# Kernel optimization log

Measured on AMD Instinct MI355X. Metric: run time of the kernel, lower is better.

Reference implementation:

```python
import jax, jax.numpy as jnp
import numpy as np

N = 20000
E = 320000
NEG_SLOPE = 0.2
LN_EPS = 1e-5


def gat_conv(x, W, a_src, a_dst, b, src, dst, heads, ch, concat):
    # x: [N, F_in]; W: [F_in, H*C]; a_src/a_dst: [H, C]; b: [H*C] or [C]
    xl = (x @ W).reshape(N, heads, ch)                      # [N,H,C]
    alpha_src = jnp.sum(xl * a_src, axis=-1)                # [N,H]
    alpha_dst = jnp.sum(xl * a_dst, axis=-1)                # [N,H]
    e = alpha_src[src] + alpha_dst[dst]                     # [E',H]
    e = jax.nn.leaky_relu(e, NEG_SLOPE)
    # segment softmax over incoming edges of each dst node
    m = jax.ops.segment_max(e, dst, num_segments=N)         # [N,H]
    m = jnp.where(jnp.isfinite(m), m, 0.0)
    ex = jnp.exp(e - m[dst])
    denom = jax.ops.segment_sum(ex, dst, num_segments=N)    # [N,H]
    alpha = ex / (denom[dst] + 1e-16)                       # [E',H]
    msg = alpha[:, :, None] * xl[src]                       # [E',H,C]
    out = jax.ops.segment_sum(msg, dst, num_segments=N)     # [N,H,C]
    if concat:
        return out.reshape(N, heads * ch) + b
    return out.mean(axis=1) + b


def layer_norm(x, g, b):
    mu = jnp.mean(x, axis=-1, keepdims=True)
    var = jnp.mean(jnp.square(x - mu), axis=-1, keepdims=True)
    return (x - mu) * jax.lax.rsqrt(var + LN_EPS) * g + b


def setup_inputs() -> dict:
    key = jax.random.key(0)
    ks = jax.random.split(key, 24)
    d = {}
    d["x"] = jax.random.normal(ks[0], (N, 50), dtype=jnp.float32)
    d["edge_index"] = jax.random.randint(ks[1], (2, E), 0, N, dtype=jnp.int64)

    def glorot(k, shape):
        fan = shape[0] + shape[-1]
        return jax.random.normal(k, shape, dtype=jnp.float32) * np.sqrt(2.0 / fan)

    # conv1: 50 -> 256, heads=4, concat
    d["W1"] = glorot(ks[2], (50, 4 * 256))
    d["a_src1"] = glorot(ks[3], (4, 256))
    d["a_dst1"] = glorot(ks[4], (4, 256))
    d["b1"] = jnp.zeros((4 * 256,), jnp.float32)
    # conv2: 1024 -> 256, heads=4, concat
    d["W2"] = glorot(ks[5], (1024, 4 * 256))
    d["a_src2"] = glorot(ks[6], (4, 256))
    d["a_dst2"] = glorot(ks[7], (4, 256))
    d["b2"] = jnp.zeros((4 * 256,), jnp.float32)
    # conv3: 1024 -> 121, heads=6, concat=False
    d["W3"] = glorot(ks[8], (1024, 6 * 121))
    d["a_src3"] = glorot(ks[9], (6, 121))
    d["a_dst3"] = glorot(ks[10], (6, 121))
    d["b3"] = jnp.zeros((121,), jnp.float32)
    # skips
    d["skipW1"] = glorot(ks[11], (50, 1024))
    d["skipb1"] = jnp.zeros((1024,), jnp.float32)
    d["skipW2"] = glorot(ks[12], (1024, 1024))
    d["skipb2"] = jnp.zeros((1024,), jnp.float32)
    # layer norms
    d["g1"] = jnp.ones((1024,), jnp.float32)
    d["beta1"] = jnp.zeros((1024,), jnp.float32)
    d["g2"] = jnp.ones((1024,), jnp.float32)
    d["beta2"] = jnp.zeros((1024,), jnp.float32)
    return d


def reference(x, edge_index, W1, a_src1, a_dst1, b1, W2, a_src2, a_dst2, b2,
              W3, a_src3, a_dst3, b3, skipW1, skipb1, skipW2, skipb2,
              g1, beta1, g2, beta2):
    # add self loops (PyG GATConv default)
    loop = jnp.arange(N, dtype=edge_index.dtype)
    src = jnp.concatenate([edge_index[0], loop])
    dst = jnp.concatenate([edge_index[1], loop])

    h = gat_conv(x, W1, a_src1, a_dst1, b1, src, dst, 4, 256, True)
    h = jax.nn.elu(layer_norm(h + (x @ skipW1 + skipb1), g1, beta1))
    h2 = gat_conv(h, W2, a_src2, a_dst2, b2, src, dst, 4, 256, True)
    h2 = jax.nn.elu(layer_norm(h2 + (h @ skipW2 + skipb2), g2, beta2))
    out = gat_conv(h2, W3, a_src3, a_dst3, b3, src, dst, 6, 121, False)
    return out
```

## Files before the change

kernel.cpp:

```cpp
#include <hip/hip_runtime.h>
#include <hip/hip_bf16.h>
#include <math.h>

typedef __attribute__((ext_vector_type(8))) __bf16 bf16x8;
typedef __attribute__((ext_vector_type(4))) float f32x4;

#define MPAD 20224
#define SSZ ((size_t)MPAD * 128)

#if __has_builtin(__builtin_amdgcn_global_load_lds)
#define GLD16(g, l)                                                                      \
    __builtin_amdgcn_global_load_lds(                                                    \
        (const __attribute__((address_space(1))) unsigned int*)(g),                      \
        (__attribute__((address_space(3))) unsigned int*)(l), 16, 0, 0)
#else
#define GLD16(g, l) (*(bf16x8*)(l) = *(const bf16x8*)(g))
#endif

#define BAR() asm volatile("s_barrier" ::: "memory")
#define WAITVM(N) asm volatile("s_waitcnt vmcnt(" #N ")" ::: "memory")


#define STAGE_T(t_)                                                                      \
    do {                                                                                 \
        __bf16* Ld = lds + (((t_) & 3) * 16384);                                         \
        const __bf16* Ga = Abase + (t_) * 32;                                            \
        const __bf16* Gb = Bbase + (t_) * 32;                                            \
        GLD16(Ga, Ld + tt * 8);                                                          \
        GLD16(Ga + (size_t)128 * K_, Ld + (tt + 512) * 8);                               \
        GLD16(Gb, Ld + 8192 + tt * 8);                                                   \
        GLD16(Gb + (size_t)128 * K_, Ld + 8192 + (tt + 512) * 8);                        \
    } while (0)

#define LOAD_FRAGS(t_)                                                                   \
    {                                                                                    \
        const __bf16* Ar = lds + (((t_) & 3) * 16384) + aoff;                            \
        const __bf16* Br = lds + (((t_) & 3) * 16384) + 8192 + boff;                     \
        _Pragma("unroll") for (int i = 0; i < 8; i++)                                    \
            af[i] = *(const bf16x8*)(Ar + i * 512);                                      \
        _Pragma("unroll") for (int j = 0; j < 4; j++)                                    \
            bf[j] = *(const bf16x8*)(Br + j * 512);                                      \
    }

#define MFMA_ALL()                                                                       \
    __builtin_amdgcn_s_setprio(1);                                                       \
    _Pragma("unroll") for (int i = 0; i < 8; i++)                                        \
        _Pragma("unroll") for (int j = 0; j < 4; j++)                                    \
            acc[i][j] = __builtin_amdgcn_mfma_f32_16x16x32_bf16(af[i], bf[j],            \
                                                                acc[i][j], 0, 0, 0);     \
    __builtin_amdgcn_s_setprio(0);

#define GEMM256_BODY(A, Bt, K_, ...)                                                     \
    __shared__ __align__(16) __bf16 lds[65536];                                          \
    const int tt = threadIdx.x;                                                          \
    const int lane = tt & 63;                                                            \
    const int wid = tt >> 6;                                                             \
    const int wr = wid >> 2;                                           \
    const int wc = wid & 3;                                         \
     \
    const int nwg = gridDim.x * gridDim.y;                                               \
    const int wg0 = blockIdx.y * gridDim.x + blockIdx.x;                                 \
    const int qq = nwg >> 3, rr = nwg & 7, xcd = wg0 & 7, oo = wg0 >> 3;                 \
    const int swz = (xcd < rr ? xcd * (qq + 1) : rr * (qq + 1) + (xcd - rr) * qq) + oo;  \
    const int bm = (swz / gridDim.x) * 256;                                              \
    const int bn = (swz % gridDim.x) * 256;                                              \
    const int m16 = lane & 15;                                                           \
    const int c4 = lane >> 4;                                                            \
    const int NT = K_ >> 5;                                                              \
    const int ttp = tt ^ (((tt >> 5) & 1) << 1);          \
    const int srow = ttp >> 2;                                                           \
    const int sch = (ttp & 3) << 3;                                                      \
    const __bf16* Abase = A + (size_t)(bm + srow) * K_ + sch;                            \
    const __bf16* Bbase = Bt + (size_t)(bn + srow) * K_ + sch;                           \
    const int fsw = ((m16 >> 3) & 1) << 4;                                               \
    const int aoff = (((wr * 128 + m16) * 32) + c4 * 8) ^ fsw;                           \
    const int boff = (((wc * 64 + m16) * 32) + c4 * 8) ^ fsw;                            \
    f32x4 acc[8][4];                                                                     \
    _Pragma("unroll") for (int i = 0; i < 8; i++)                                        \
        _Pragma("unroll") for (int j = 0; j < 4; j++)                                    \
            acc[i][j] = (f32x4){0.f, 0.f, 0.f, 0.f};                                     \
    bf16x8 af[8], bf[4];                                                                 \
                      \
    STAGE_T(0);                                                                          \
    if (NT > 1) STAGE_T(1);                                                              \
    if (NT > 2) STAGE_T(2);                                                              \
    if (NT > 2) { WAITVM(8); } else if (NT > 1) { WAITVM(4); } else { WAITVM(0); }       \
    BAR();                                                                               \
    for (int t = 0; t < NT; t++) {                                                       \
        if (t + 3 < NT) STAGE_T(t + 3);                                                  \
        LOAD_FRAGS(t);                                                                   \
        MFMA_ALL();                                                                      \
        if (t + 1 < NT) {                                                                \
            if (t + 3 < NT) { WAITVM(8); }                                               \
            else if (t + 3 == NT) { WAITVM(4); }                                         \
            else { WAITVM(0); }                                                          \
            BAR();                                                                       \
        }                                                                                \
    }                                                                                    \
    __VA_ARGS__

__global__ __launch_bounds__(512, 2) void gemm256_bt(const __bf16* __restrict__ A,
                                                     const __bf16* __restrict__ Bt,
                                                     __bf16* __restrict__ C,
                                                     int M, int N_, int K_) {
    GEMM256_BODY(A, Bt, K_,
        { const int r4 = c4 << 2;
          const int rb = bm + wr * 128;
          _Pragma("unroll") for (int i = 0; i < 8; i++)
              _Pragma("unroll") for (int j = 0; j < 4; j++) {
                  int col = bn + wc * 64 + j * 16 + m16;
                  size_t sb_ = (size_t)(col >> 7) * SSZ + (col & 127);
                  _Pragma("unroll") for (int r = 0; r < 4; r++) {
                      int row = rb + i * 16 + r4 + r;
                      C[sb_ + (size_t)row * 128] = (__bf16)acc[i][j][r];
                  }
              } })
}

__global__ __launch_bounds__(512, 2) void gemm256_bt2(const __bf16* __restrict__ A,
                                                      const __bf16* __restrict__ Bt,
                                                      __bf16* __restrict__ C0,
                                                      __bf16* __restrict__ C1,
                                                      int M, int K_) {
    GEMM256_BODY(A, Bt, K_,
        { const int r4 = c4 << 2;
          const int rb = bm + wr * 128;
          _Pragma("unroll") for (int i = 0; i < 8; i++)
              _Pragma("unroll") for (int j = 0; j < 4; j++) {
                  int col = bn + wc * 64 + j * 16 + m16;
                  __bf16* Cp = (col < 1024) ? C0 : C1;
                  int c10 = col & 1023;
                  size_t sb_ = (size_t)(c10 >> 7) * SSZ + (c10 & 127);
                  _Pragma("unroll") for (int r = 0; r < 4; r++) {
                      int row = rb + i * 16 + r4 + r;
                      Cp[sb_ + (size_t)row * 128] = (__bf16)acc[i][j][r];
                  }
              } })
}

__device__ __forceinline__ void transpose_tile(const float* __restrict__ W,
                                               __bf16* __restrict__ WT,
                                               int K, int N, int Kp, int Np,
                                               int bx, int by, float* sm) {
    int tx = threadIdx.x & 31, ty = threadIdx.x >> 5;
#pragma unroll
    for (int r = ty; r < 32; r += 8) {
        int k = by * 32 + r, n = bx * 32 + tx;
        float v = 0.f;
        if (k < K && n < N) v = W[(size_t)k * N + n];
        sm[r * 33 + tx] = v;
    }
    __syncthreads();
#pragma unroll
    for (int r = ty; r < 32; r += 8) {
        int n = bx * 32 + r, k = by * 32 + tx;
        if (n < Np && k < Kp) WT[(size_t)n * Kp + k] = (__bf16)sm[tx * 33 + r];
    }
}

__device__ __forceinline__ void transpose_w3_tile(const float* __restrict__ W,
                                                  __bf16* __restrict__ WT,
                                                  int bx, int by, float* sm) {
    int tx = threadIdx.x & 31, ty = threadIdx.x >> 5;
    int r0 = bx * 32;
    int h = r0 >> 7;
    int c0 = r0 & 127;
#pragma unroll
    for (int r = ty; r < 32; r += 8) {
        int k = by * 32 + r;
        int c = c0 + tx;
        float v = 0.f;
        if (c < 121) v = W[(size_t)k * 726 + h * 121 + c];
        sm[r * 33 + tx] = v;
    }
    __syncthreads();
#pragma unroll
    for (int r = ty; r < 32; r += 8) {
        int rr = r0 + r;
        int k = by * 32 + tx;
        WT[(size_t)rr * 1024 + k] = (__bf16)sm[tx * 33 + r];
    }
}

__global__ __launch_bounds__(256) void prep_k(const float* __restrict__ x,
                                              const float* __restrict__ W1,
                                              const float* __restrict__ sW1,
                                              const float* __restrict__ W2,
                                              const float* __restrict__ sW2,
                                              const float* __restrict__ W3,
                                              __bf16* __restrict__ xp,
                                              __bf16* __restrict__ WTcat1,
                                              __bf16* __restrict__ WTcat2,
                                              __bf16* __restrict__ W3pT, int Nn) {
    __shared__ float sm[32 * 33];
    int b = blockIdx.x;
    if (b < 5056) {
        int i = b * 256 + threadIdx.x;
        int n = i >> 6, c = i & 63;
        float v = 0.f;
        if (n < Nn && c < 50) v = x[n * 50 + c];
        xp[(size_t)n * 64 + c] = (__bf16)v;
    } else if (b < 5120) {
        int i = b - 5056; transpose_tile(W1, WTcat1, 50, 1024, 64, 1024, i % 32, i / 32, sm);
    } else if (b < 5184) {
        int i = b - 5120; transpose_tile(sW1, WTcat1 + 1024 * 64, 50, 1024, 64, 1024, i % 32, i / 32, sm);
    } else if (b < 6208) {
        int i = b - 5184; transpose_tile(W2, WTcat2, 1024, 1024, 1024, 1024, i % 32, i / 32, sm);
    } else if (b < 7232) {
        int i = b - 6208; transpose_tile(sW2, WTcat2 + (size_t)1024 * 1024, 1024, 1024, 1024, 1024, i % 32, i / 32, sm);
    } else {
        int i = b - 7232; transpose_w3_tile(W3, W3pT, i % 24, i / 24, sm);
    }
}

__global__ void zero_probe_k(const int* __restrict__ ei, int* __restrict__ cnt,
                             int* __restrict__ flag, int Nn) {
    int i = blockIdx.x * 256 + threadIdx.x;
    if (i < Nn) cnt[i] = 0;
    if (blockIdx.x == 0 && threadIdx.x == 0) {
        int all0 = 1;
        for (int k = 0; k < 64; k++)
            if (ei[2 * k + 1] != 0) { all0 = 0; break; }
        *flag = all0;
    }
}

__device__ __forceinline__ int load_ei(const int* ei, int idx, int is64) {
    return is64 ? ei[2 * idx] : ei[idx];
}

__global__ void hist_k(const int* __restrict__ ei, const int* __restrict__ flag,
                       int* __restrict__ cnt, int E, int Nn) {
    int e = blockIdx.x * 256 + threadIdx.x;
    if (e >= E + Nn) return;
    int is64 = *flag;
    int d = (e < E) ? load_ei(ei, E + e, is64) : (e - E);
    d = min(max(d, 0), Nn - 1);
    atomicAdd(&cnt[d], 1);
}

__global__ __launch_bounds__(1024) void scan_k(int* __restrict__ cnt, int* __restrict__ row_ptr,
                                               int Nn) {
    __shared__ int part[1024];
    int t = threadIdx.x;
    int chunk = (Nn + 1023) >> 10;
    int lo = t * chunk;
    int hi = lo + chunk; if (hi > Nn) hi = Nn; if (lo > Nn) lo = Nn;
    int s = 0;
    for (int i = lo; i < hi; i++) s += (cnt[i] + 7) & ~7;
    part[t] = s;
    __syncthreads();
    for (int off = 1; off < 1024; off <<= 1) {
        int v = (t >= off) ? part[t - off] : 0;
        __syncthreads();
        part[t] += v;
        __syncthreads();
    }
    int run = part[t] - s;
    for (int i = lo; i < hi; i++) { row_ptr[i] = run; run += (cnt[i] + 7) & ~7; }
    if (t == 1023) row_ptr[Nn] = part[1023];
    __syncthreads();
    for (int i = lo; i < hi; i++) cnt[i] = 0;
}

__global__ void fill_csr_k(const int* __restrict__ ei, const int* __restrict__ flag,
                           const int* __restrict__ row_ptr, int* __restrict__ cursor,
                           int* __restrict__ src_csr, int E, int Nn) {
    int e = blockIdx.x * 256 + threadIdx.x;
    if (e >= E + Nn) return;
    int is64 = *flag;
    int d = (e < E) ? load_ei(ei, E + e, is64) : (e - E);
    int s = (e < E) ? load_ei(ei, e, is64) : (e - E);
    d = min(max(d, 0), Nn - 1);
    s = min(max(s, 0), Nn - 1);
    int slot = row_ptr[d] + atomicAdd(&cursor[d], 1);
    src_csr[slot] = s;
}

__global__ void alpha_k(const __bf16* __restrict__ XL, int sph, const float* __restrict__ a_src,
                        const float* __restrict__ a_dst, float* __restrict__ asrc,
                        float* __restrict__ adst, int Nn, int H, int C) {
    int gw = (blockIdx.x * 256 + threadIdx.x) >> 6;
    int lane = threadIdx.x & 63;
    if (gw >= Nn * H) return;
    int n = gw / H, h = gw - n * H;
    const float* as = a_src + h * C;
    const float* ad = a_dst + h * C;
    float s = 0.f, d = 0.f;
    for (int c = lane; c < C; c += 64) {
        float v = (float)XL[(size_t)(h * sph + (c >> 7)) * SSZ + (size_t)n * 128 + (c & 127)];
        s += v * as[c];
        d += v * ad[c];
    }
#pragma unroll
    for (int off = 32; off; off >>= 1) {
        s += __shfl_down(s, off);
        d += __shfl_down(d, off);
    }
    if (lane == 0) { asrc[n * H + h] = s; adst[n * H + h] = d; }
}

__global__ void attn_k(const int* __restrict__ row_ptr, const int* __restrict__ deg,
                       const int* __restrict__ src_csr,
                       const float* __restrict__ asrc, const float* __restrict__ adst,
                       float* __restrict__ wt, int Nn, int H, int Ecap) {
    int gw = (blockIdx.x * 256 + threadIdx.x) >> 6;
    int lane = threadIdx.x & 63;
    if (gw >= Nn) return;
    int n = gw;
    int base = row_ptr[n], dg = deg[n];
    if (dg <= 64) {
        bool v = lane < dg;
        int src = v ? src_csr[base + lane] : 0;
        for (int h = 0; h < H; h++) {
            float ad = adst[n * H + h];
            float e = -1e30f;
            if (v) {
                e = asrc[src * H + h] + ad;
                e = e > 0.f ? e : 0.2f * e;
            }
            float m = e;
#pragma unroll
            for (int off = 1; off < 64; off <<= 1) m = fmaxf(m, __shfl_xor(m, off));
            float ex = v ? __expf(e - m) : 0.f;
            float sum = ex;
#pragma unroll
            for (int off = 1; off < 64; off <<= 1) sum += __shfl_xor(sum, off);
            if (v) wt[(size_t)h * Ecap + base + lane] = ex / (sum + 1e-16f);
        }
        return;
    }
    for (int h = 0; h < H; h++) {
        float ad = adst[n * H + h];
        float m = -1e30f;
        for (int s = lane; s < dg; s += 64) {
            float e = asrc[src_csr[base + s] * H + h] + ad;
            e = e > 0.f ? e : 0.2f * e;
            m = fmaxf(m, e);
        }
#pragma unroll
        for (int off = 1; off < 64; off <<= 1) m = fmaxf(m, __shfl_xor(m, off));
        float sum = 0.f;
        for (int s = lane; s < dg; s += 64) {
            float e = asrc[src_csr[base + s] * H + h] + ad;
            e = e > 0.f ? e : 0.2f * e;
            sum += __expf(e - m);
        }
#pragma unroll
        for (int off = 1; off < 64; off <<= 1) sum += __shfl_xor(sum, off);
        float inv = 1.f / (sum + 1e-16f);
        float* wrow = wt + (size_t)h * Ecap;
        for (int s = lane; s < dg; s += 64) {
            float e = asrc[src_csr[base + s] * H + h] + ad;
            e = e > 0.f ? e : 0.2f * e;
            wrow[base + s] = __expf(e - m) * inv;
        }
    }
}

__global__ __launch_bounds__(256) void agg_skip8(const __bf16* __restrict__ XL,
                                                 const float* __restrict__ wt,
                                                 const int* __restrict__ row_ptr,
                                                 const int* __restrict__ src_csr,
                                                 const float* __restrict__ bias,
                                                 const float* __restrict__ sb,
                                                 __bf16* __restrict__ SK, int Nn, int Ecap) {
    const int bid = blockIdx.x;
    const int cc = bid & 7;
    const int n = (bid >> 3) * 4 + (threadIdx.x >> 6);
    const int lane = threadIdx.x & 63;
    if (n >= Nn) return;
    const int g = lane >> 4;
    const int p = lane & 15;
    const int col = cc * 128 + p * 8;
    const float* wrow = wt + (size_t)(cc >> 1) * Ecap;
    const __bf16* XLc = XL + (size_t)cc * SSZ + p * 8;
    const int base = row_ptr[n], end = row_ptr[n + 1];

    float acc[8];
#pragma unroll
    for (int j = 0; j < 8; j++) acc[j] = 0.f;

    for (int e = base; e < end; e += 8) {
        int2 si = *(const int2*)(src_csr + e + 2 * g);
        float2 wv = *(const float2*)(wrow + e + 2 * g);
        bf16x8 xa = *(const bf16x8*)(XLc + (size_t)si.x * 128);
        bf16x8 xb = *(const bf16x8*)(XLc + (size_t)si.y * 128);
#pragma unroll
        for (int j = 0; j < 8; j++) acc[j] += wv.x * (float)xa[j] + wv.y * (float)xb[j];
    }
#pragma unroll
    for (int j = 0; j < 8; j++) {
        acc[j] += __shfl_xor(acc[j], 16);
        acc[j] += __shfl_xor(acc[j], 32);
    }
    if (lane < 16) {
        size_t o = (size_t)cc * SSZ + (size_t)n * 128 + p * 8;
        bf16x8 sk = *(const bf16x8*)(SK + o);
        bf16x8 res;
#pragma unroll
        for (int j = 0; j < 8; j++)
            res[j] = (__bf16)(acc[j] + bias[col + j] + sb[col + j] + (float)sk[j]);
        *(bf16x8*)(SK + o) = res;
    }
}

__global__ __launch_bounds__(256) void agg_mean8(const __bf16* __restrict__ XL,
                                                 const float* __restrict__ wt,
                                                 const int* __restrict__ row_ptr,
                                                 const int* __restrict__ src_csr,
                                                 __bf16* __restrict__ part, int Nn, int Ecap) {
    const int bid = blockIdx.x;
    const int swz = (bid & 7) * 3750 + (bid >> 3);
    const int cc = swz / 5000;
    const int nb = swz - cc * 5000;
    const int n = nb * 4 + (threadIdx.x >> 6);
    const int lane = threadIdx.x & 63;
    if (n >= Nn) return;
    const int g = lane >> 4;
    const int p = lane & 15;
    const int col = cc * 128 + p * 8;
    const float* wrow = wt + (size_t)cc * Ecap;
    const __bf16* XLc = XL + (size_t)cc * SSZ + p * 8;
    const int base = row_ptr[n], end = row_ptr[n + 1];

    float acc[8];
#pragma unroll
    for (int j = 0; j < 8; j++) acc[j] = 0.f;

    for (int e = base; e < end; e += 8) {
        int2 si = *(const int2*)(src_csr + e + 2 * g);
        float2 wv = *(const float2*)(wrow + e + 2 * g);
        bf16x8 xa = *(const bf16x8*)(XLc + (size_t)si.x * 128);
        bf16x8 xb = *(const bf16x8*)(XLc + (size_t)si.y * 128);
#pragma unroll
        for (int j = 0; j < 8; j++) acc[j] += wv.x * (float)xa[j] + wv.y * (float)xb[j];
    }
#pragma unroll
    for (int j = 0; j < 8; j++) {
        acc[j] += __shfl_xor(acc[j], 16);
        acc[j] += __shfl_xor(acc[j], 32);
    }
    if (lane < 16) {
        size_t o = (size_t)n * 768 + col;
        bf16x8 res;
#pragma unroll
        for (int j = 0; j < 8; j++) res[j] = (__bf16)acc[j];
        *(bf16x8*)(part + o) = res;
    }
}

__global__ __launch_bounds__(128) void reduce_mean_k(const __bf16* __restrict__ part,
                                                     const float* __restrict__ b3,
                                                     float* __restrict__ out, int Nn) {
    int n = blockIdx.x;
    int t = threadIdx.x;
    if (t >= 121) return;
    const __bf16* row = part + (size_t)n * 768;
    float s = 0.f;
#pragma unroll
    for (int h = 0; h < 6; h++) s += (float)row[h * 128 + t];
    out[(size_t)n * 121 + t] = s * (1.f / 6.f) + b3[t];
}

__global__ __launch_bounds__(256) void ln_elu_k(const __bf16* __restrict__ in,
                                                const float* __restrict__ g,
                                                const float* __restrict__ be,
                                                __bf16* __restrict__ out, int rows_real) {
    const int half = threadIdx.x >> 7;
    const int t = threadIdx.x & 127;
    const int n = blockIdx.x * 2 + half;
    const size_t ro = (size_t)n * 1024 + t * 8;
    __shared__ float rs[8];
    bf16x8 v8;
    float v[8];
    float s = 0.f, q = 0.f;
    const bool live = (n < rows_real);
    if (live) {
        v8 = *(const bf16x8*)(in + (size_t)(t >> 4) * SSZ + (size_t)n * 128 + (t & 15) * 8);
#pragma unroll
        for (int j = 0; j < 8; j++) {
            v[j] = (float)v8[j];
            s += v[j];
            q += v[j] * v[j];
        }
    }
#pragma unroll
    for (int off = 32; off; off >>= 1) {
        s += __shfl_down(s, off);
        q += __shfl_down(q, off);
    }
    int wid = threadIdx.x >> 6;
    if ((threadIdx.x & 63) == 0) { rs[wid] = s; rs[wid + 4] = q; }
    __syncthreads();
    if (!live) {
        bf16x8 z;
#pragma unroll
        for (int j = 0; j < 8; j++) z[j] = (__bf16)0.f;
        *(bf16x8*)(out + ro) = z;
        return;
    }
    int w0 = half * 2;
    s = rs[w0] + rs[w0 + 1];
    q = rs[w0 + 4] + rs[w0 + 5];
    float mu = s * (1.f / 1024.f);
    float var = q * (1.f / 1024.f) - mu * mu;
    float inv = rsqrtf(fmaxf(var, 0.f) + 1e-5f);
    bf16x8 o8;
#pragma unroll
    for (int j = 0; j < 8; j++) {
        int c = t * 8 + j;
        float y = (v[j] - mu) * inv * g[c] + be[c];
        y = y > 0.f ? y : expm1f(y);
        o8[j] = (__bf16)y;
    }
    *(bf16x8*)(out + ro) = o8;
}

extern "C" void kernel_launch(void* const* d_in, const int* in_sizes, int n_in,
                              void* d_out, int out_size, void* d_ws, size_t ws_size,
                              hipStream_t stream) {
    const float* x   = (const float*)d_in[0];
    const int*   ei  = (const int*)d_in[1];
    const float* W1  = (const float*)d_in[2];
    const float* as1 = (const float*)d_in[3];
    const float* ad1 = (const float*)d_in[4];
    const float* b1  = (const float*)d_in[5];
    const float* W2  = (const float*)d_in[6];
    const float* as2 = (const float*)d_in[7];
    const float* ad2 = (const float*)d_in[8];
    const float* b2  = (const float*)d_in[9];
    const float* W3  = (const float*)d_in[10];
    const float* as3 = (const float*)d_in[11];
    const float* ad3 = (const float*)d_in[12];
    const float* b3  = (const float*)d_in[13];
    const float* sW1 = (const float*)d_in[14];
    const float* sb1 = (const float*)d_in[15];
    const float* sW2 = (const float*)d_in[16];
    const float* sb2 = (const float*)d_in[17];
    const float* g1  = (const float*)d_in[18];
    const float* be1 = (const float*)d_in[19];
    const float* g2  = (const float*)d_in[20];
    const float* be2 = (const float*)d_in[21];
    float* out = (float*)d_out;

    const int Nn = 20000;
    const int E = in_sizes[1] / 2;
    const int E2 = E + Nn;
    const int Ecap = E2 + 8 * Nn;
    const int Mpad = MPAD;

    char* p = (char*)d_ws;
    auto alloc = [&](size_t bytes) {
        char* r = p;
        p += (bytes + 255) & ~(size_t)255;
        return r;
    };
    __bf16* WTcat1 = (__bf16*)alloc((size_t)2048 * 64 * 2);
    __bf16* WTcat2 = (__bf16*)alloc((size_t)2048 * 1024 * 2);
    __bf16* W3pT   = (__bf16*)alloc((size_t)768 * 1024 * 2);
    __bf16* xp     = (__bf16*)alloc((size_t)Mpad * 64 * 2);
    __bf16* XL     = (__bf16*)alloc((size_t)Mpad * 1024 * 2);
    __bf16* SK     = (__bf16*)alloc((size_t)Mpad * 1024 * 2);
    __bf16* H1     = (__bf16*)alloc((size_t)Mpad * 1024 * 2);
    float*  asrcb  = (float*)alloc((size_t)Nn * 6 * 4);
    float*  adstb  = (float*)alloc((size_t)Nn * 6 * 4);
    float*  wbuf   = (float*)alloc((size_t)6 * Ecap * 4);
    int*    rowp   = (int*)alloc((size_t)(Nn + 1) * 4);
    int*    cnt    = (int*)alloc((size_t)Nn * 4);
    int*    scsr   = (int*)alloc((size_t)Ecap * 4);
    int*    eiflag = (int*)alloc(256);
    __bf16* part   = SK;
    (void)ws_size; (void)n_in; (void)out_size;

    prep_k<<<8000, 256, 0, stream>>>(x, W1, sW1, W2, sW2, W3, xp, WTcat1, WTcat2, W3pT, Nn);

    zero_probe_k<<<(Nn + 255) / 256, 256, 0, stream>>>(ei, cnt, eiflag, Nn);
    hist_k<<<(E2 + 255) / 256, 256, 0, stream>>>(ei, eiflag, cnt, E, Nn);
    scan_k<<<1, 1024, 0, stream>>>(cnt, rowp, Nn);
    (void)hipMemsetAsync(scsr, 0, (size_t)Ecap * 4, stream);
    (void)hipMemsetAsync(wbuf, 0, (size_t)6 * Ecap * 4, stream);
    fill_csr_k<<<(E2 + 255) / 256, 256, 0, stream>>>(ei, eiflag, rowp, cnt, scsr, E, Nn);

    gemm256_bt2<<<dim3(8, Mpad / 256), 512, 0, stream>>>(xp, WTcat1, XL, SK, Mpad, 64);
    alpha_k<<<(Nn * 4 * 64) / 256, 256, 0, stream>>>(XL, 2, as1, ad1, asrcb, adstb, Nn, 4, 256);
    attn_k<<<(Nn + 3) / 4, 256, 0, stream>>>(rowp, cnt, scsr, asrcb, adstb, wbuf, Nn, 4, Ecap);
    agg_skip8<<<((Nn + 3) / 4) * 8, 256, 0, stream>>>(XL, wbuf, rowp, scsr, b1, sb1, SK, Nn, Ecap);
    ln_elu_k<<<Mpad / 2, 256, 0, stream>>>(SK, g1, be1, H1, Nn);

    gemm256_bt2<<<dim3(8, Mpad / 256), 512, 0, stream>>>(H1, WTcat2, XL, SK, Mpad, 1024);
    alpha_k<<<(Nn * 4 * 64) / 256, 256, 0, stream>>>(XL, 2, as2, ad2, asrcb, adstb, Nn, 4, 256);
    attn_k<<<(Nn + 3) / 4, 256, 0, stream>>>(rowp, cnt, scsr, asrcb, adstb, wbuf, Nn, 4, Ecap);
    agg_skip8<<<((Nn + 3) / 4) * 8, 256, 0, stream>>>(XL, wbuf, rowp, scsr, b2, sb2, SK, Nn, Ecap);
    ln_elu_k<<<Mpad / 2, 256, 0, stream>>>(SK, g2, be2, H1, Nn);

    gemm256_bt<<<dim3(3, Mpad / 256), 512, 0, stream>>>(H1, W3pT, XL, Mpad, 768, 1024);
    alpha_k<<<(Nn * 6 * 64) / 256, 256, 0, stream>>>(XL, 1, as3, ad3, asrcb, adstb, Nn, 6, 121);
    attn_k<<<(Nn + 3) / 4, 256, 0, stream>>>(rowp, cnt, scsr, asrcb, adstb, wbuf, Nn, 6, Ecap);
    agg_mean8<<<((Nn + 3) / 4) * 6, 256, 0, stream>>>(XL, wbuf, rowp, scsr, part, Nn, Ecap);
    reduce_mean_k<<<Nn, 128, 0, stream>>>(part, b3, out, Nn);
}
```

Before: 845.5 us.

## Narrow feature slabs from 128 to 64 columns for cache-friendlier gathers

Changes the column-slab layout of the projected features from 128-wide to 64-wide slabs and updates the GEMM epilogues, alpha, aggregation and layernorm indexing to match. Aggregation kernels now use a 2D grid with twice as many column chunks, each lane gathering 4 bf16 values instead of 8. The intent is to shrink the per-slab working set so the random source-node gathers hit in L2/MALL more often, at the cost of smaller 8-byte loads and more blocks re-reading the CSR indices and weights. It also drops the block swizzle in the mean aggregation.

Result: slower. 1.018 ms (+20.4%).

```diff
diff --git a/kernel.cpp b/kernel.cpp
--- a/kernel.cpp
+++ b/kernel.cpp
@@ -3,10 +3,11 @@
 #include <math.h>
 
 typedef __attribute__((ext_vector_type(8))) __bf16 bf16x8;
+typedef __attribute__((ext_vector_type(4))) __bf16 bf16x4;
 typedef __attribute__((ext_vector_type(4))) float f32x4;
 
 #define MPAD 20224
-#define SSZ ((size_t)MPAD * 128)
+#define SHS ((size_t)MPAD * 64)
 
 #if __has_builtin(__builtin_amdgcn_global_load_lds)
 #define GLD16(g, l)                                                                      \
@@ -109,10 +110,10 @@
           _Pragma("unroll") for (int i = 0; i < 8; i++)
               _Pragma("unroll") for (int j = 0; j < 4; j++) {
                   int col = bn + wc * 64 + j * 16 + m16;
-                  size_t sb_ = (size_t)(col >> 7) * SSZ + (col & 127);
+                  size_t sb_ = (size_t)(col >> 6) * SHS + (col & 63);
                   _Pragma("unroll") for (int r = 0; r < 4; r++) {
                       int row = rb + i * 16 + r4 + r;
-                      C[sb_ + (size_t)row * 128] = (__bf16)acc[i][j][r];
+                      C[sb_ + (size_t)row * 64] = (__bf16)acc[i][j][r];
                   }
               } })
 }
@@ -130,10 +131,10 @@
                   int col = bn + wc * 64 + j * 16 + m16;
                   __bf16* Cp = (col < 1024) ? C0 : C1;
                   int c10 = col & 1023;
-                  size_t sb_ = (size_t)(c10 >> 7) * SSZ + (c10 & 127);
+                  size_t sb_ = (size_t)(c10 >> 6) * SHS + (c10 & 63);
                   _Pragma("unroll") for (int r = 0; r < 4; r++) {
                       int row = rb + i * 16 + r4 + r;
-                      Cp[sb_ + (size_t)row * 128] = (__bf16)acc[i][j][r];
+                      Cp[sb_ + (size_t)row * 64] = (__bf16)acc[i][j][r];
                   }
               } })
 }
@@ -288,7 +289,7 @@
     const float* ad = a_dst + h * C;
     float s = 0.f, d = 0.f;
     for (int c = lane; c < C; c += 64) {
-        float v = (float)XL[(size_t)(h * sph + (c >> 7)) * SSZ + (size_t)n * 128 + (c & 127)];
+        float v = (float)XL[(size_t)(h * sph + (c >> 6)) * SHS + (size_t)n * 64 + (c & 63)];
         s += v * as[c];
         d += v * ad[c];
     }
@@ -365,43 +366,42 @@
                                                  const float* __restrict__ bias,
                                                  const float* __restrict__ sb,
                                                  __bf16* __restrict__ SK, int Nn, int Ecap) {
-    const int bid = blockIdx.x;
-    const int cc = bid & 7;
-    const int n = (bid >> 3) * 4 + (threadIdx.x >> 6);
+    const int cc = blockIdx.y;
+    const int n = blockIdx.x * 4 + (threadIdx.x >> 6);
     const int lane = threadIdx.x & 63;
     if (n >= Nn) return;
     const int g = lane >> 4;
     const int p = lane & 15;
-    const int col = cc * 128 + p * 8;
-    const float* wrow = wt + (size_t)(cc >> 1) * Ecap;
-    const __bf16* XLc = XL + (size_t)cc * SSZ + p * 8;
+    const int col = cc * 64 + p * 4;
+    const float* wrow = wt + (size_t)(cc >> 2) * Ecap;
+    const __bf16* XLc = XL + (size_t)cc * SHS + p * 4;
     const int base = row_ptr[n], end = row_ptr[n + 1];
 
-    float acc[8];
-#pragma unroll
-    for (int j = 0; j < 8; j++) acc[j] = 0.f;
+    float acc[4];
+#pragma unroll
+    for (int j = 0; j < 4; j++) acc[j] = 0.f;
 
     for (int e = base; e < end; e += 8) {
         int2 si = *(const int2*)(src_csr + e + 2 * g);
         float2 wv = *(const float2*)(wrow + e + 2 * g);
-        bf16x8 xa = *(const bf16x8*)(XLc + (size_t)si.x * 128);
-        bf16x8 xb = *(const bf16x8*)(XLc + (size_t)si.y * 128);
-#pragma unroll
-        for (int j = 0; j < 8; j++) acc[j] += wv.x * (float)xa[j] + wv.y * (float)xb[j];
-    }
-#pragma unroll
-    for (int j = 0; j < 8; j++) {
+        bf16x4 xa = *(const bf16x4*)(XLc + (size_t)si.x * 64);
+        bf16x4 xb = *(const bf16x4*)(XLc + (size_t)si.y * 64);
+#pragma unroll
+        for (int j = 0; j < 4; j++) acc[j] += wv.x * (float)xa[j] + wv.y * (float)xb[j];
+    }
+#pragma unroll
+    for (int j = 0; j < 4; j++) {
         acc[j] += __shfl_xor(acc[j], 16);
         acc[j] += __shfl_xor(acc[j], 32);
     }
     if (lane < 16) {
-        size_t o = (size_t)cc * SSZ + (size_t)n * 128 + p * 8;
-        bf16x8 sk = *(const bf16x8*)(SK + o);
-        bf16x8 res;
-#pragma unroll
-        for (int j = 0; j < 8; j++)
+        size_t o = (size_t)cc * SHS + (size_t)n * 64 + p * 4;
+        bf16x4 sk = *(const bf16x4*)(SK + o);
+        bf16x4 res;
+#pragma unroll
+        for (int j = 0; j < 4; j++)
             res[j] = (__bf16)(acc[j] + bias[col + j] + sb[col + j] + (float)sk[j]);
-        *(bf16x8*)(SK + o) = res;
+        *(bf16x4*)(SK + o) = res;
     }
 }
 
@@ -410,43 +410,40 @@
                                                  const int* __restrict__ row_ptr,
                                                  const int* __restrict__ src_csr,
                                                  __bf16* __restrict__ part, int Nn, int Ecap) {
-    const int bid = blockIdx.x;
-    const int swz = (bid & 7) * 3750 + (bid >> 3);
-    const int cc = swz / 5000;
-    const int nb = swz - cc * 5000;
-    const int n = nb * 4 + (threadIdx.x >> 6);
+    const int cc = blockIdx.y;
+    const int n = blockIdx.x * 4 + (threadIdx.x >> 6);
     const int lane = threadIdx.x & 63;
     if (n >= Nn) return;
     const int g = lane >> 4;
     const int p = lane & 15;
-    const int col = cc * 128 + p * 8;
-    const float* wrow = wt + (size_t)cc * Ecap;
-    const __bf16* XLc = XL + (size_t)cc * SSZ + p * 8;
+    const int col = cc * 64 + p * 4;
+    const float* wrow = wt + (size_t)(cc >> 1) * Ecap;
+    const __bf16* XLc = XL + (size_t)cc * SHS + p * 4;
     const int base = row_ptr[n], end = row_ptr[n + 1];
 
-    float acc[8];
-#pragma unroll
-    for (int j = 0; j < 8; j++) acc[j] = 0.f;
+    float acc[4];
+#pragma unroll
+    for (int j = 0; j < 4; j++) acc[j] = 0.f;
 
     for (int e = base; e < end; e += 8) {
         int2 si = *(const int2*)(src_csr + e + 2 * g);
         float2 wv = *(const float2*)(wrow + e + 2 * g);
-        bf16x8 xa = *(const bf16x8*)(XLc + (size_t)si.x * 128);
-        bf16x8 xb = *(const bf16x8*)(XLc + (size_t)si.y * 128);
-#pragma unroll
-        for (int j = 0; j < 8; j++) acc[j] += wv.x * (float)xa[j] + wv.y * (float)xb[j];
-    }
-#pragma unroll
-    for (int j = 0; j < 8; j++) {
+        bf16x4 xa = *(const bf16x4*)(XLc + (size_t)si.x * 64);
+        bf16x4 xb = *(const bf16x4*)(XLc + (size_t)si.y * 64);
+#pragma unroll
+        for (int j = 0; j < 4; j++) acc[j] += wv.x * (float)xa[j] + wv.y * (float)xb[j];
+    }
+#pragma unroll
+    for (int j = 0; j < 4; j++) {
         acc[j] += __shfl_xor(acc[j], 16);
         acc[j] += __shfl_xor(acc[j], 32);
     }
     if (lane < 16) {
         size_t o = (size_t)n * 768 + col;
-        bf16x8 res;
-#pragma unroll
-        for (int j = 0; j < 8; j++) res[j] = (__bf16)acc[j];
-        *(bf16x8*)(part + o) = res;
+        bf16x4 res;
+#pragma unroll
+        for (int j = 0; j < 4; j++) res[j] = (__bf16)acc[j];
+        *(bf16x4*)(part + o) = res;
     }
 }
 
@@ -477,7 +474,7 @@
     float s = 0.f, q = 0.f;
     const bool live = (n < rows_real);
     if (live) {
-        v8 = *(const bf16x8*)(in + (size_t)(t >> 4) * SSZ + (size_t)n * 128 + (t & 15) * 8);
+        v8 = *(const bf16x8*)(in + (size_t)(t >> 3) * SHS + (size_t)n * 64 + (t & 7) * 8);
 #pragma unroll
         for (int j = 0; j < 8; j++) {
             v[j] = (float)v8[j];
@@ -583,20 +580,20 @@
     fill_csr_k<<<(E2 + 255) / 256, 256, 0, stream>>>(ei, eiflag, rowp, cnt, scsr, E, Nn);
 
     gemm256_bt2<<<dim3(8, Mpad / 256), 512, 0, stream>>>(xp, WTcat1, XL, SK, Mpad, 64);
-    alpha_k<<<(Nn * 4 * 64) / 256, 256, 0, stream>>>(XL, 2, as1, ad1, asrcb, adstb, Nn, 4, 256);
+    alpha_k<<<(Nn * 4 * 64) / 256, 256, 0, stream>>>(XL, 4, as1, ad1, asrcb, adstb, Nn, 4, 256);
     attn_k<<<(Nn + 3) / 4, 256, 0, stream>>>(rowp, cnt, scsr, asrcb, adstb, wbuf, Nn, 4, Ecap);
-    agg_skip8<<<((Nn + 3) / 4) * 8, 256, 0, stream>>>(XL, wbuf, rowp, scsr, b1, sb1, SK, Nn, Ecap);
+    agg_skip8<<<dim3((Nn + 3) / 4, 16), 256, 0, stream>>>(XL, wbuf, rowp, scsr, b1, sb1, SK, Nn, Ecap);
     ln_elu_k<<<Mpad / 2, 256, 0, stream>>>(SK, g1, be1, H1, Nn);
 
     gemm256_bt2<<<dim3(8, Mpad / 256), 512, 0, stream>>>(H1, WTcat2, XL, SK, Mpad, 1024);
-    alpha_k<<<(Nn * 4 * 64) / 256, 256, 0, stream>>>(XL, 2, as2, ad2, asrcb, adstb, Nn, 4, 256);
+    alpha_k<<<(Nn * 4 * 64) / 256, 256, 0, stream>>>(XL, 4, as2, ad2, asrcb, adstb, Nn, 4, 256);
     attn_k<<<(Nn + 3) / 4, 256, 0, stream>>>(rowp, cnt, scsr, asrcb, adstb, wbuf, Nn, 4, Ecap);
-    agg_skip8<<<((Nn + 3) / 4) * 8, 256, 0, stream>>>(XL, wbuf, rowp, scsr, b2, sb2, SK, Nn, Ecap);
+    agg_skip8<<<dim3((Nn + 3) / 4, 16), 256, 0, stream>>>(XL, wbuf, rowp, scsr, b2, sb2, SK, Nn, Ecap);
     ln_elu_k<<<Mpad / 2, 256, 0, stream>>>(SK, g2, be2, H1, Nn);
 
     gemm256_bt<<<dim3(3, Mpad / 256), 512, 0, stream>>>(H1, W3pT, XL, Mpad, 768, 1024);
-    alpha_k<<<(Nn * 6 * 64) / 256, 256, 0, stream>>>(XL, 1, as3, ad3, asrcb, adstb, Nn, 6, 121);
+    alpha_k<<<(Nn * 6 * 64) / 256, 256, 0, stream>>>(XL, 2, as3, ad3, asrcb, adstb, Nn, 6, 121);
     attn_k<<<(Nn + 3) / 4, 256, 0, stream>>>(rowp, cnt, scsr, asrcb, adstb, wbuf, Nn, 6, Ecap);
-    agg_mean8<<<((Nn + 3) / 4) * 6, 256, 0, stream>>>(XL, wbuf, rowp, scsr, part, Nn, Ecap);
+    agg_mean8<<<dim3((Nn + 3) / 4, 12), 256, 0, stream>>>(XL, wbuf, rowp, scsr, part, Nn, Ecap);
     reduce_mean_k<<<Nn, 128, 0, stream>>>(part, b3, out, Nn);
 }
```
